# Performance work log

Measured on AMD Instinct MI355X. Metric: run time of the kernel, lower is better.

The kernel has to match this reference:

```python
import jax, jax.numpy as jnp
import numpy as np

B, T_FRAMES, N, D, H, HT = 2, 16, 256, 768, 12, 12
INNER = 2 * D  # ConditionedTransitionBlock expansion_factor=2

def _ln(x, eps=1e-5):
    m = jnp.mean(x, axis=-1, keepdims=True)
    v = jnp.var(x, axis=-1, keepdims=True)
    return (x - m) * jax.lax.rsqrt(v + eps)

def _adaln(a, s, snorm_w, scale_w, scale_b, shift_w):
    an = _ln(a)            # LayerNorm(dim), no affine
    sn = _ln(s) * snorm_w  # LayerNorm(dim_cond), weight only
    return jax.nn.sigmoid(sn @ scale_w + scale_b) * an + sn @ shift_w

def _forward(a, s, bias, timestamps,
             ada_snorm_w, ada_scale_w, ada_scale_b, ada_shift_w,
             pb_q_w, pb_q_b, pb_k_w, pb_v_w, pb_g_w, pb_o_w,
             op_w, op_b,
             tr_snorm_w, tr_scale_w, tr_scale_b, tr_shift_w,
             tr_gate_w, tr_ab_w, tr_ba_w, tr_out_w, tr_out_b,
             tmp_ln_w, tmp_ln_b, tmp_q_w, tmp_q_b, tmp_k_w, tmp_v_w,
             tmp_decay, tmp_o_w,
             mask, multiplicity, T):
    BT, Nn, Dd = a.shape
    Bb = BT // T
    dh = Dd // H
    # --- AdaLN ---
    b = _adaln(a, s, ada_snorm_w, ada_scale_w, ada_scale_b, ada_shift_w)
    # --- pair-bias spatial attention (compute_pair_bias=False: z already (B,N,N,H)) ---
    q = (b @ pb_q_w + pb_q_b).reshape(BT, Nn, H, dh)
    k = (b @ pb_k_w).reshape(BT, Nn, H, dh)
    v = (b @ pb_v_w).reshape(BT, Nn, H, dh)
    z = jnp.transpose(bias, (0, 3, 1, 2))     # (B, H, N, N)
    z = jnp.repeat(z, multiplicity, axis=0)   # expand over T -> (B*T, H, N, N)
    scores = jnp.einsum('bqhd,bkhd->bhqk', q, k) * (dh ** -0.5) + z
    scores = jnp.where(mask[:, None, None, :], scores, -1e6)
    attn = jax.nn.softmax(scores, axis=-1)
    o = jnp.einsum('bhqk,bkhd->bqhd', attn, v).reshape(BT, Nn, Dd)
    g = jax.nn.sigmoid(b @ pb_g_w)
    attn_out = (g * o) @ pb_o_w
    # gated output projection (sigmoid, weights init 0 / bias -2) multiplied into residual
    a = a + jax.nn.sigmoid(s @ op_w + op_b) * attn_out
    # --- temporal attention with decay over T frames ---
    x = a.reshape(Bb, T, Nn, Dd).transpose(0, 2, 1, 3)   # (B, N, T, D)
    h = _ln(x) * tmp_ln_w + tmp_ln_b
    dht = Dd // HT
    qt = (h @ tmp_q_w + tmp_q_b).reshape(Bb, Nn, T, HT, dht)
    kt = (h @ tmp_k_w).reshape(Bb, Nn, T, HT, dht)
    vt = (h @ tmp_v_w).reshape(Bb, Nn, T, HT, dht)
    dt = jnp.abs(timestamps[:, :, None] - timestamps[:, None, :])           # (B, T, T)
    tb = -jax.nn.softplus(tmp_decay)[None, :, None, None] * dt[:, None]     # (B, HT, T, T)
    sct = jnp.einsum('bnqhd,bnkhd->bnhqk', qt, kt) * (dht ** -0.5) + tb[:, None]
    att = jax.nn.softmax(sct, axis=-1)
    ot = jnp.einsum('bnhqk,bnkhd->bnqhd', att, vt).reshape(Bb, Nn, T, Dd) @ tmp_o_w
    x = x + ot  # residual inside temporal attention
    a = x.transpose(0, 2, 1, 3).reshape(BT, Nn, Dd)
    # --- conditioned transition (SwiGLU gated by sigmoid(Linear(s))) ---
    b2 = _adaln(a, s, tr_snorm_w, tr_scale_w, tr_scale_b, tr_shift_w)
    hid = jax.nn.silu(b2 @ tr_gate_w) * (b2 @ tr_ab_w)
    a = a + jax.nn.sigmoid(s @ tr_out_w + tr_out_b) * (hid @ tr_ba_w)
    return a  # post_layer_norm=False -> Identity

def setup_inputs():
    key = jax.random.key(0)
    ks = iter(jax.random.split(key, 48))
    f = lambda shape, sc=1.0: jax.random.normal(next(ks), shape, jnp.float32) * sc
    return {
        'a': f((B * T_FRAMES, N, D)),
        's': f((B * T_FRAMES, N, D)),
        'bias': f((B, N, N, H)),
        'mask': jnp.ones((B * T_FRAMES, N), dtype=bool),
        'timestamps': jnp.sort(jax.random.uniform(next(ks), (B, T_FRAMES)) * 10.0, axis=-1),
        'multiplicity': T_FRAMES,
        'T': T_FRAMES,
        'ada_snorm_w': jnp.ones((D,)), 'ada_scale_w': f((D, D), 0.02),
        'ada_scale_b': jnp.zeros((D,)), 'ada_shift_w': f((D, D), 0.02),
        'pb_q_w': f((D, D), 0.02), 'pb_q_b': jnp.zeros((D,)),
        'pb_k_w': f((D, D), 0.02), 'pb_v_w': f((D, D), 0.02),
        'pb_g_w': f((D, D), 0.02), 'pb_o_w': f((D, D), 0.02),
        'op_w': f((D, D), 0.02), 'op_b': jnp.full((D,), -2.0),
        'tr_snorm_w': jnp.ones((D,)), 'tr_scale_w': f((D, D), 0.02),
        'tr_scale_b': jnp.zeros((D,)), 'tr_shift_w': f((D, D), 0.02),
        'tr_gate_w': f((D, INNER), 0.02), 'tr_ab_w': f((D, INNER), 0.02),
        'tr_ba_w': f((INNER, D), 0.02),
        'tr_out_w': f((D, D), 0.02), 'tr_out_b': jnp.full((D,), -2.0),
        'tmp_ln_w': jnp.ones((D,)), 'tmp_ln_b': jnp.zeros((D,)),
        'tmp_q_w': f((D, D), 0.02), 'tmp_q_b': jnp.zeros((D,)),
        'tmp_k_w': f((D, D), 0.02), 'tmp_v_w': f((D, D), 0.02),
        'tmp_decay': jnp.full((HT,), 0.5), 'tmp_o_w': f((D, D), 0.02),
    }

def reference(a, s, bias, mask, timestamps, multiplicity, T,
              ada_snorm_w, ada_scale_w, ada_scale_b, ada_shift_w,
              pb_q_w, pb_q_b, pb_k_w, pb_v_w, pb_g_w, pb_o_w,
              op_w, op_b,
              tr_snorm_w, tr_scale_w, tr_scale_b, tr_shift_w,
              tr_gate_w, tr_ab_w, tr_ba_w, tr_out_w, tr_out_b,
              tmp_ln_w, tmp_ln_b, tmp_q_w, tmp_q_b, tmp_k_w, tmp_v_w,
              tmp_decay, tmp_o_w):
    return _forward(a, s, bias, timestamps,
                    ada_snorm_w, ada_scale_w, ada_scale_b, ada_shift_w,
                    pb_q_w, pb_q_b, pb_k_w, pb_v_w, pb_g_w, pb_o_w,
                    op_w, op_b,
                    tr_snorm_w, tr_scale_w, tr_scale_b, tr_shift_w,
                    tr_gate_w, tr_ab_w, tr_ba_w, tr_out_w, tr_out_b,
                    tmp_ln_w, tmp_ln_b, tmp_q_w, tmp_q_b, tmp_k_w, tmp_v_w,
                    tmp_decay, tmp_o_w,
                    mask, multiplicity, T)
```

## Files before the change

### kernel.cpp

```cpp
#include <hip/hip_runtime.h>

typedef short s16x8 __attribute__((ext_vector_type(8)));
typedef short s16x4 __attribute__((ext_vector_type(4)));
typedef float f32x4 __attribute__((ext_vector_type(4)));
typedef __bf16 bf16x8 __attribute__((ext_vector_type(8)));

__device__ __forceinline__ float bf2f(short u) {
  union { unsigned int i; float f; } c;
  c.i = ((unsigned int)(unsigned short)u) << 16;
  return c.f;
}
__device__ __forceinline__ short f2bf(float f) {
  union { float f; unsigned int i; } c; c.f = f;
  unsigned int r = c.i + 0x7FFFu + ((c.i >> 16) & 1u);
  return (short)(r >> 16);
}
__device__ __forceinline__ float sigmoidf_(float x) { return 1.f / (1.f + __expf(-x)); }

template <typename T>
__device__ __forceinline__ auto mfma_sel(T a, T b, f32x4 c, int)
    -> decltype(__builtin_amdgcn_mfma_f32_16x16x32_bf16(a, b, c, 0, 0, 0)) {
  return __builtin_amdgcn_mfma_f32_16x16x32_bf16(a, b, c, 0, 0, 0);
}
template <typename T>
__device__ __forceinline__ f32x4 mfma_sel(T a, T b, f32x4 c, long) {
  return __builtin_amdgcn_mfma_f32_16x16x32_bf16(
      __builtin_bit_cast(bf16x8, a), __builtin_bit_cast(bf16x8, b), c, 0, 0, 0);
}
__device__ __forceinline__ f32x4 MFMA16(s16x8 a, s16x8 b, f32x4 c) {
  return mfma_sel(a, b, c, 0);
}

__device__ __forceinline__ void gl2lds16(const void* g, void* l) {
  __builtin_amdgcn_global_load_lds(
      (const __attribute__((address_space(1))) unsigned int*)g,
      (__attribute__((address_space(3))) unsigned int*)l, 16, 0, 0);
}

#define OFF_WADA1    0u
#define OFF_WQKVG    2359296u
#define OFF_WO       7077888u
#define OFF_WGATES   8257536u
#define OFF_WTMPQKV  10616832u
#define OFF_WTMPO    14155776u
#define OFF_WADA2    15335424u
#define OFF_WTRANS   17694720u
#define OFF_WBA      22413312u
#define OFF_BIAS     24772608u
#define OFF_ZT       24812544u
#define OFF_AN1      31104000u
#define OFF_SN1      43686912u
#define OFF_SN2      56269824u
#define OFF_SBF      68852736u
#define OFF_CADA     81435648u
#define OFF_QKVG     106601472u
#define OFF_GATES    156933120u
#define OFF_OGO      182098944u
#define OFF_A1       194681856u

__global__ __launch_bounds__(256) void prep_all(
    const float* p0, const float* p1, const float* p2, const float* p3,
    const float* p4, const float* p5, const float* p6, const float* p7,
    const float* p8, const float* p9, const float* p10, const float* p11,
    const float* p12, const float* p13, const float* p14, const float* p15,
    const float* p16, const float* p17, short* wsb,
    const float* __restrict__ zsrc, const float* __restrict__ ada_scale_b,
    const float* __restrict__ pb_q_b, const float* __restrict__ op_b,
    const float* __restrict__ tr_out_b, const float* __restrict__ tmp_q_b,
    const float* __restrict__ tr_scale_b,
    float* __restrict__ biasbuf, short* __restrict__ zt,
    const float* __restrict__ a_in, const float* __restrict__ s_in,
    const float* __restrict__ lnw1, const float* __restrict__ lnw2,
    short* __restrict__ an1, short* __restrict__ sn1, short* __restrict__ sn2,
    short* __restrict__ sbf) {
  const int z = blockIdx.z;
  const int tid = threadIdx.y * 32 + threadIdx.x;
  if (z < 18) {
    struct E { int K, N, dst; };
    const E tab[18] = {
        {768, 768, 0},        {768, 768, 589824},
        {768, 768, 1179648},  {768, 768, 1769472},
        {768, 768, 2359296},  {768, 768, 2949120},
        {768, 768, 3538944},
        {768, 768, 4128768},  {768, 768, 4718592},
        {768, 768, 7667712},  {768, 768, 8257536},
        {768, 1536, 8847360}, {768, 1536, 10027008},
        {1536, 768, 11206656},
        {768, 768, 5308416},  {768, 768, 5898240}, {768, 768, 6488064},
        {768, 768, 7077888}};
    int K = tab[z].K, N = tab[z].N;
    int n0 = blockIdx.x << 5, k0 = blockIdx.y << 5;
    if (n0 >= N || k0 >= K) return;
    const float* src;
    switch (z) {
      case 0: src = p0; break;  case 1: src = p1; break;
      case 2: src = p2; break;  case 3: src = p3; break;
      case 4: src = p4; break;  case 5: src = p5; break;
      case 6: src = p6; break;  case 7: src = p7; break;
      case 8: src = p8; break;  case 9: src = p9; break;
      case 10: src = p10; break; case 11: src = p11; break;
      case 12: src = p12; break; case 13: src = p13; break;
      case 14: src = p14; break; case 15: src = p15; break;
      case 16: src = p16; break; default: src = p17; break;
    }
    short* dst = wsb + tab[z].dst;
    __shared__ float tile[32][33];
    int tx = threadIdx.x, ty = threadIdx.y;
#pragma unroll
    for (int j = 0; j < 4; j++)
      tile[ty + j * 8][tx] = src[(long)(k0 + ty + j * 8) * N + n0 + tx];
    __syncthreads();
#pragma unroll
    for (int j = 0; j < 4; j++)
      dst[(long)(n0 + ty + j * 8) * K + k0 + tx] = f2bf(tile[tx][ty + j * 8]);
  } else if (z == 18) {
    const int bid = blockIdx.y * 48 + blockIdx.x;
    if (bid < 512) {
      const int b = bid >> 8, qq = bid & 255;
      const float* src = zsrc + (long)bid * 3072 + tid * 12;
      f32x4 v0 = *(const f32x4*)(src);
      f32x4 v1 = *(const f32x4*)(src + 4);
      f32x4 v2 = *(const f32x4*)(src + 8);
      float vals[12] = {v0[0], v0[1], v0[2], v0[3], v1[0], v1[1],
                        v1[2], v1[3], v2[0], v2[1], v2[2], v2[3]};
#pragma unroll
      for (int h = 0; h < 12; h++)
        zt[(((long)(b * 12 + h) * 256 + qq) << 8) + tid] = f2bf(vals[h]);
    } else if (bid < 551) {
      int j = (bid - 512) * 256 + tid;
      if (j < 9984) {
        float v;
        if (j < 1536) v = (j < 768) ? ada_scale_b[j] : 0.f;
        else if (j < 4608) { int jj = j - 1536; v = (jj < 768) ? pb_q_b[jj] : 0.f; }
        else if (j < 6144) { int jj = j - 4608; v = (jj < 768) ? op_b[jj] : tr_out_b[jj - 768]; }
        else if (j < 8448) { int jj = j - 6144; v = (jj < 768) ? tmp_q_b[jj] : 0.f; }
        else { int jj = j - 8448; v = (jj < 768) ? tr_scale_b[jj] : 0.f; }
        biasbuf[j] = v;
      }
    }
  } else {
    const int bid = blockIdx.y * 48 + blockIdx.x;
    if (bid >= 2048) return;
    const int wave = tid >> 6, lane = tid & 63;
    const int row = (bid << 2) + wave;
    const float* ar = a_in + (long)row * 768;
    const float* sr = s_in + (long)row * 768;
    f32x4 av[3], sv[3];
    float s0 = 0, s1 = 0, s2 = 0, s3 = 0;
#pragma unroll
    for (int k = 0; k < 3; k++) {
      int col = (lane << 2) + (k << 8);
      av[k] = *(const f32x4*)(ar + col);
      sv[k] = *(const f32x4*)(sr + col);
#pragma unroll
      for (int e = 0; e < 4; e++) {
        s0 += av[k][e]; s1 += av[k][e] * av[k][e];
        s2 += sv[k][e]; s3 += sv[k][e] * sv[k][e];
      }
    }
#pragma unroll
    for (int o = 32; o; o >>= 1) {
      s0 += __shfl_xor(s0, o, 64); s1 += __shfl_xor(s1, o, 64);
      s2 += __shfl_xor(s2, o, 64); s3 += __shfl_xor(s3, o, 64);
    }
    const float inv768 = 1.f / 768.f;
    float ma = s0 * inv768, va = s1 * inv768 - ma * ma;
    float ia = rsqrtf(va + 1e-5f);
    float ms = s2 * inv768, vs = s3 * inv768 - ms * ms;
    float is_ = rsqrtf(vs + 1e-5f);
#pragma unroll
    for (int k = 0; k < 3; k++) {
      int col = (lane << 2) + (k << 8);
      long o = (long)row * 768 + col;
      s16x4 o1, o2, o3, o4;
#pragma unroll
      for (int e = 0; e < 4; e++) {
        o1[e] = f2bf((av[k][e] - ma) * ia);
        float sn = (sv[k][e] - ms) * is_;
        o2[e] = f2bf(sn * lnw1[col + e]);
        o3[e] = f2bf(sn * lnw2[col + e]);
        o4[e] = f2bf(sv[k][e]);
      }
      *(s16x4*)(an1 + o) = o1;
      *(s16x4*)(sn1 + o) = o2;
      *(s16x4*)(sn2 + o) = o3;
      *(s16x4*)(sbf + o) = o4;
    }
  }
}

__global__ __launch_bounds__(256) void ln_affine(
    const float* __restrict__ in, const float* __restrict__ w,
    const float* __restrict__ b, short* __restrict__ out) {
  const int wave = threadIdx.x >> 6, lane = threadIdx.x & 63;
  const int row = (blockIdx.x << 2) + wave;
  const float* xr = in + (long)row * 768;
  f32x4 xv[3];
  float s0 = 0, s1 = 0;
#pragma unroll
  for (int k = 0; k < 3; k++) {
    int col = (lane << 2) + (k << 8);
    xv[k] = *(const f32x4*)(xr + col);
#pragma unroll
    for (int e = 0; e < 4; e++) { s0 += xv[k][e]; s1 += xv[k][e] * xv[k][e]; }
  }
#pragma unroll
  for (int o = 32; o; o >>= 1) { s0 += __shfl_xor(s0, o, 64); s1 += __shfl_xor(s1, o, 64); }
  const float inv768 = 1.f / 768.f;
  float m = s0 * inv768, v = s1 * inv768 - m * m;
  float inv = rsqrtf(v + 1e-5f);
#pragma unroll
  for (int k = 0; k < 3; k++) {
    int col = (lane << 2) + (k << 8);
    s16x4 p;
#pragma unroll
    for (int e = 0; e < 4; e++) {
      float y = (xv[k][e] - m) * inv;
      if (w) y = y * w[col + e] + b[col + e];
      p[e] = f2bf(y);
    }
    *(s16x4*)(out + (long)row * 768 + col) = p;
  }
}

template <int EP>
__device__ __forceinline__ void dev_gemm_bt(
    short* lds,
    const short* __restrict__ A, const short* __restrict__ W,
    const float* __restrict__ bias, void* __restrict__ Cout,
    const float* __restrict__ res, const short* __restrict__ gate,
    int K, int ldA, int ldC, int gld) {
  short* sA = lds;
  short* sB = lds + 8192;
  const int tid = threadIdx.x;
  const int wave = tid >> 6;
  const int lane = tid & 63;
  const int m0 = blockIdx.y << 7;
  const int n0 = blockIdx.x << 7;
  const int wm = (wave & 1) << 6, wn = (wave >> 1) << 6;
  const int q = lane >> 4, r = lane & 15;
  f32x4 acc[4][4];
#pragma unroll
  for (int i = 0; i < 4; i++)
#pragma unroll
    for (int j = 0; j < 4; j++) acc[i][j] = (f32x4){0.f, 0.f, 0.f, 0.f};

  for (int kt = 0; kt < K; kt += 64) {
    __syncthreads();
#pragma unroll
    for (int t = 0; t < 4; t++) {
      int c = (t << 8) + tid;
      int m = c >> 3, kc = (c & 7) ^ (m & 7);
      gl2lds16(A + (long)(m0 + m) * ldA + kt + (kc << 3),
               sA + (((t << 8) + (wave << 6)) << 3));
    }
#pragma unroll
    for (int t = 0; t < 4; t++) {
      int c = (t << 8) + tid;
      int m = c >> 3, kc = (c & 7) ^ (m & 7);
      gl2lds16(W + (long)(n0 + m) * K + kt + (kc << 3),
               sB + (((t << 8) + (wave << 6)) << 3));
    }
    __syncthreads();
#pragma unroll
    for (int ks = 0; ks < 2; ks++) {
      s16x8 av[4], bv[4];
#pragma unroll
      for (int mt = 0; mt < 4; mt++) {
        int row = wm + (mt << 4) + r;
        int ch = ((ks << 2) + q) ^ (row & 7);
        av[mt] = *(const s16x8*)(sA + ((row << 3) + ch) * 8);
      }
#pragma unroll
      for (int nt = 0; nt < 4; nt++) {
        int row = wn + (nt << 4) + r;
        int ch = ((ks << 2) + q) ^ (row & 7);
        bv[nt] = *(const s16x8*)(sB + ((row << 3) + ch) * 8);
      }
#pragma unroll
      for (int mt = 0; mt < 4; mt++)
#pragma unroll
        for (int nt = 0; nt < 4; nt++)
          acc[mt][nt] = MFMA16(bv[nt], av[mt], acc[mt][nt]);
    }
  }
#pragma unroll
  for (int mt = 0; mt < 4; mt++) {
    const int gm = m0 + wm + (mt << 4) + r;
#pragma unroll
    for (int nt = 0; nt < 4; nt++) {
      const int gnb = n0 + wn + (nt << 4) + (q << 2);
      f32x4 v = acc[mt][nt];
      if (bias) {
        f32x4 b4 = *(const f32x4*)(bias + gnb);
        v += b4;
      }
      long o = (long)gm * ldC + gnb;
      if (EP == 0) {
        s16x4 p;
#pragma unroll
        for (int e = 0; e < 4; e++) p[e] = f2bf(v[e]);
        *(s16x4*)((short*)Cout + o) = p;
      } else if (EP == 1) {
        s16x4 p;
#pragma unroll
        for (int e = 0; e < 4; e++) p[e] = f2bf(sigmoidf_(v[e]));
        *(s16x4*)((short*)Cout + o) = p;
      } else if (EP == 2) {
        f32x4 r4 = *(const f32x4*)(res + o);
        *(f32x4*)((float*)Cout + o) = r4 + v;
      } else {
        f32x4 r4 = *(const f32x4*)(res + o);
        s16x4 g4 = *(const s16x4*)(gate + (long)gm * gld + gnb);
        f32x4 out;
#pragma unroll
        for (int e = 0; e < 4; e++) out[e] = r4[e] + bf2f(g4[e]) * v[e];
        *(f32x4*)((float*)Cout + o) = out;
      }
    }
  }
}

template <int MODE>
__device__ __forceinline__ void dev_gemm_dual(
    short* lds,
    const short* __restrict__ A, const short* __restrict__ W, int woff2,
    const float* __restrict__ bias, const short* __restrict__ an,
    short* __restrict__ out, int ldO) {
  short* sA = lds;
  short* sB1 = lds + 8192;
  short* sB2 = lds + 12288;
  const int tid = threadIdx.x;
  const int wave = tid >> 6, lane = tid & 63;
  const int m0 = blockIdx.y << 7;
  const int n0 = blockIdx.x << 6;
  const int wm = (wave & 1) << 6, wn = (wave >> 1) << 5;
  const int q = lane >> 4, r = lane & 15;
  f32x4 acc1[4][2], acc2[4][2];
#pragma unroll
  for (int i = 0; i < 4; i++)
#pragma unroll
    for (int j = 0; j < 2; j++) {
      acc1[i][j] = (f32x4){0.f, 0.f, 0.f, 0.f};
      acc2[i][j] = (f32x4){0.f, 0.f, 0.f, 0.f};
    }

  for (int kt = 0; kt < 768; kt += 64) {
    __syncthreads();
#pragma unroll
    for (int t = 0; t < 4; t++) {
      int c = (t << 8) + tid;
      int m = c >> 3, kc = (c & 7) ^ (m & 7);
      gl2lds16(A + (long)(m0 + m) * 768 + kt + (kc << 3),
               sA + (((t << 8) + (wave << 6)) << 3));
    }
#pragma unroll
    for (int t = 0; t < 2; t++) {
      int c = (t << 8) + tid;
      int m = c >> 3, kc = (c & 7) ^ (m & 7);
      gl2lds16(W + (long)(n0 + m) * 768 + kt + (kc << 3),
               sB1 + (((t << 8) + (wave << 6)) << 3));
      gl2lds16(W + (long)(woff2 + n0 + m) * 768 + kt + (kc << 3),
               sB2 + (((t << 8) + (wave << 6)) << 3));
    }
    __syncthreads();
#pragma unroll
    for (int ks = 0; ks < 2; ks++) {
      s16x8 av[4], b1[2], b2[2];
#pragma unroll
      for (int mt = 0; mt < 4; mt++) {
        int row = wm + (mt << 4) + r;
        int ch = ((ks << 2) + q) ^ (row & 7);
        av[mt] = *(const s16x8*)(sA + ((row << 3) + ch) * 8);
      }
#pragma unroll
      for (int nt = 0; nt < 2; nt++) {
        int row = wn + (nt << 4) + r;
        int ch = ((ks << 2) + q) ^ (row & 7);
        b1[nt] = *(const s16x8*)(sB1 + ((row << 3) + ch) * 8);
        b2[nt] = *(const s16x8*)(sB2 + ((row << 3) + ch) * 8);
      }
#pragma unroll
      for (int mt = 0; mt < 4; mt++)
#pragma unroll
        for (int nt = 0; nt < 2; nt++) {
          acc1[mt][nt] = MFMA16(b1[nt], av[mt], acc1[mt][nt]);
          acc2[mt][nt] = MFMA16(b2[nt], av[mt], acc2[mt][nt]);
        }
    }
  }
#pragma unroll
  for (int mt = 0; mt < 4; mt++) {
    const int gm = m0 + wm + (mt << 4) + r;
#pragma unroll
    for (int nt = 0; nt < 2; nt++) {
      const int gnb = n0 + wn + (nt << 4) + (q << 2);
      s16x4 p;
      if (MODE == 0) {
        f32x4 b4 = *(const f32x4*)(bias + gnb);
        s16x4 an4 = *(const s16x4*)(an + (long)gm * 768 + gnb);
#pragma unroll
        for (int e = 0; e < 4; e++)
          p[e] = f2bf(sigmoidf_(acc1[mt][nt][e] + b4[e]) * bf2f(an4[e]) +
                      acc2[mt][nt][e]);
      } else {
#pragma unroll
        for (int e = 0; e < 4; e++) {
          float x = acc1[mt][nt][e];
          p[e] = f2bf(x * sigmoidf_(x) * acc2[mt][nt][e]);
        }
      }
      *(s16x4*)(out + (long)gm * ldO + gnb) = p;
    }
  }
}

template <int EP>
__global__ __launch_bounds__(256) void gemm_bt(
    const short* __restrict__ A, const short* __restrict__ W,
    const float* __restrict__ bias, void* __restrict__ Cout,
    const float* __restrict__ res, const short* __restrict__ gate,
    int K, int ldA, int ldC, int gld) {
  __shared__ short lds[16384];
  dev_gemm_bt<EP>(lds, A, W, bias, Cout, res, gate, K, ldA, ldC, gld);
}

template <int MODE>
__global__ __launch_bounds__(256) void gemm_dual(
    const short* __restrict__ A, const short* __restrict__ W, int woff2,
    const float* __restrict__ bias, const short* __restrict__ an,
    short* __restrict__ out, int ldO) {
  __shared__ short lds[16384];
  dev_gemm_dual<MODE>(lds, A, W, woff2, bias, an, out, ldO);
}

__global__ __launch_bounds__(256) void gemm_pair(
    const short* __restrict__ sbf, const short* __restrict__ wgates,
    const float* __restrict__ bias_g, short* __restrict__ gates,
    const short* __restrict__ sn1, const short* __restrict__ wada1,
    const float* __restrict__ bias_a, const short* __restrict__ an1,
    short* __restrict__ outb) {
  __shared__ short lds[16384];
  if (blockIdx.z == 0)
    dev_gemm_bt<1>(lds, sbf, wgates, bias_g, (void*)gates, nullptr, nullptr,
                   768, 768, 1536, 0);
  else
    dev_gemm_dual<0>(lds, sn1, wada1, 768, bias_a, an1, outb, 768);
}

__global__ __launch_bounds__(256) void attn_spatial(
    const short* __restrict__ qkvg, const short* __restrict__ zt, short* __restrict__ ogo) {
  __shared__ short sKP[256 * 64];
  __shared__ short sVt[64 * 256];
  const int tid = threadIdx.x;
  const int wave = tid >> 6, lane = tid & 63;
  const int qt = blockIdx.x, h = blockIdx.y, bt = blockIdx.z;
  const int b = bt >> 4;
  const int q0 = qt << 6;
  const long rowbase = (long)bt << 8;
  const int hoff = h << 6;

#pragma unroll
  for (int t = 0; t < 8; t++) {
    int c = (t << 8) + tid;
    int tok = c >> 3, kc = (c & 7) ^ (tok & 7);
    *(s16x8*)(sKP + (c << 3)) =
        *(const s16x8*)(qkvg + (rowbase + tok) * 3072 + 768 + hoff + (kc << 3));
  }
#pragma unroll
  for (int t = 0; t < 8; t++) {
    int u = (t << 8) + tid;
    int tok = u >> 3, dc = u & 7;
    s16x8 v8 = *(const s16x8*)(qkvg + (rowbase + tok) * 3072 + 1536 + hoff + (dc << 3));
#pragma unroll
    for (int e = 0; e < 8; e++) {
      int d = (dc << 3) + e;
      int ch = (tok >> 3) ^ (d & 7);
      sVt[((d << 5) + ch) * 8 + (tok & 7)] = v8[e];
    }
  }
  __syncthreads();

  const int q = lane >> 4, cc = lane & 15;
  f32x4 acc[16];
#pragma unroll
  for (int i = 0; i < 16; i++) acc[i] = (f32x4){0.f, 0.f, 0.f, 0.f};
  {
    const int arow = (wave << 4) + cc;
    const short* qrow = qkvg + (rowbase + q0 + arow) * 3072 + hoff;
#pragma unroll
    for (int ks = 0; ks < 2; ks++) {
      s16x8 av = *(const s16x8*)(qrow + (ks << 5) + (q << 3));
#pragma unroll
      for (int nt = 0; nt < 16; nt++) {
        int tok = (nt << 4) + cc;
        int chb = ((ks << 2) + q) ^ (tok & 7);
        s16x8 bv = *(const s16x8*)(sKP + ((tok << 3) + chb) * 8);
        acc[nt] = MFMA16(av, bv, acc[nt]);
      }
    }
  }
  const short* ztb = zt + (((long)(b * 12 + h) * 256 + q0 + (wave << 4)) << 8);
#pragma unroll
  for (int reg = 0; reg < 4; reg++) {
    int lr = (q << 2) + reg;
    float mx = -3.0e38f;
#pragma unroll
    for (int nt = 0; nt < 16; nt++) {
      float v = acc[nt][reg] * 0.125f + bf2f(ztb[lr * 256 + (nt << 4) + cc]);
      acc[nt][reg] = v;
      mx = fmaxf(mx, v);
    }
    mx = fmaxf(mx, __shfl_xor(mx, 1, 16));
    mx = fmaxf(mx, __shfl_xor(mx, 2, 16));
    mx = fmaxf(mx, __shfl_xor(mx, 4, 16));
    mx = fmaxf(mx, __shfl_xor(mx, 8, 16));
    float sum = 0.f;
#pragma unroll
    for (int nt = 0; nt < 16; nt++) {
      float e = __expf(acc[nt][reg] - mx);
      acc[nt][reg] = e; sum += e;
    }
    sum += __shfl_xor(sum, 1, 16);
    sum += __shfl_xor(sum, 2, 16);
    sum += __shfl_xor(sum, 4, 16);
    sum += __shfl_xor(sum, 8, 16);
    float inv = 1.f / sum;
#pragma unroll
    for (int nt = 0; nt < 16; nt++) acc[nt][reg] *= inv;
  }
  __syncthreads();
#pragma unroll
  for (int nt = 0; nt < 16; nt++) {
#pragma unroll
    for (int reg = 0; reg < 4; reg++) {
      int rP = (wave << 4) + (q << 2) + reg;
      int col = (nt << 4) + cc;
      int ch = (col >> 3) ^ (rP & 7);
      sKP[((rP << 5) + ch) * 8 + (col & 7)] = f2bf(acc[nt][reg]);
    }
  }
  __syncthreads();
  f32x4 oacc[4];
#pragma unroll
  for (int i = 0; i < 4; i++) oacc[i] = (f32x4){0.f, 0.f, 0.f, 0.f};
  const int prow = (wave << 4) + cc;
#pragma unroll
  for (int ksi = 0; ksi < 8; ksi++) {
    int cha = ((ksi << 2) + q) ^ (prow & 7);
    s16x8 pa = *(const s16x8*)(sKP + ((prow << 5) + cha) * 8);
#pragma unroll
    for (int dt = 0; dt < 4; dt++) {
      int d = (dt << 4) + cc;
      int chv = ((ksi << 2) + q) ^ (d & 7);
      s16x8 bv = *(const s16x8*)(sVt + ((d << 5) + chv) * 8);
      oacc[dt] = MFMA16(pa, bv, oacc[dt]);
    }
  }
#pragma unroll
  for (int dt = 0; dt < 4; dt++) {
#pragma unroll
    for (int reg = 0; reg < 4; reg++) {
      int rowt = q0 + (wave << 4) + (q << 2) + reg;
      int dcol = (dt << 4) + cc;
      long grow = rowbase + rowt;
      float gl = bf2f(qkvg[grow * 3072 + 2304 + hoff + dcol]);
      ogo[grow * 768 + hoff + dcol] = f2bf(oacc[dt][reg] * sigmoidf_(gl));
    }
  }
}

__global__ __launch_bounds__(256) void attn_temporal(
    const short* __restrict__ qkvt, const float* __restrict__ ts,
    const float* __restrict__ decay_raw, short* __restrict__ out) {
  __shared__ short sKV[16 * 1544];
  const int bn = blockIdx.x;
  const int b = bn >> 8, n = bn & 255;
  const int tid = threadIdx.x;
#pragma unroll
  for (int t = 0; t < 12; t++) {
    int u = t * 256 + tid;
    int row = u / 192, cc = u % 192;
    *(s16x8*)(sKV + row * 1544 + cc * 8) =
        *(const s16x8*)(qkvt + ((long)(b * 16 + row) * 256 + n) * 2304 + 768 + cc * 8);
  }
  __syncthreads();
  const int h = tid >> 4, tq = tid & 15;
  if (h < 12) {
    const int hoff = h << 6;
    float dec = log1pf(__expf(decay_raw[h]));
    float tsq = ts[b * 16 + tq];
    s16x8 qv[8];
    const short* qrow = qkvt + ((long)(b * 16 + tq) * 256 + n) * 2304 + hoff;
#pragma unroll
    for (int dc = 0; dc < 8; dc++) qv[dc] = *(const s16x8*)(qrow + dc * 8);
    float sc[16];
#pragma unroll
    for (int tk = 0; tk < 16; tk++) {
      float dot = 0.f;
#pragma unroll
      for (int dc = 0; dc < 8; dc++) {
        s16x8 kv = *(const s16x8*)(sKV + tk * 1544 + hoff + dc * 8);
#pragma unroll
        for (int e = 0; e < 8; e++) dot += bf2f(qv[dc][e]) * bf2f(kv[e]);
      }
      sc[tk] = dot * 0.125f - dec * fabsf(tsq - ts[b * 16 + tk]);
    }
    float mx = sc[0];
#pragma unroll
    for (int tk = 1; tk < 16; tk++) mx = fmaxf(mx, sc[tk]);
    float sum = 0.f;
#pragma unroll
    for (int tk = 0; tk < 16; tk++) { sc[tk] = __expf(sc[tk] - mx); sum += sc[tk]; }
    float inv = 1.f / sum;
    float oa[64];
#pragma unroll
    for (int d = 0; d < 64; d++) oa[d] = 0.f;
#pragma unroll
    for (int tk = 0; tk < 16; tk++) {
      float wgt = sc[tk] * inv;
#pragma unroll
      for (int dc = 0; dc < 8; dc++) {
        s16x8 vv = *(const s16x8*)(sKV + tk * 1544 + 768 + hoff + dc * 8);
#pragma unroll
        for (int e = 0; e < 8; e++) oa[dc * 8 + e] += wgt * bf2f(vv[e]);
      }
    }
    long orow = (long)(b * 16 + tq) * 256 + n;
#pragma unroll
    for (int dc = 0; dc < 8; dc++) {
      s16x8 o8;
#pragma unroll
      for (int e = 0; e < 8; e++) o8[e] = f2bf(oa[dc * 8 + e]);
      *(s16x8*)(out + orow * 768 + hoff + dc * 8) = o8;
    }
  }
}

extern "C" void kernel_launch(void* const* d_in, const int* in_sizes, int n_in,
                              void* d_out, int out_size, void* d_ws, size_t ws_size,
                              hipStream_t stream) {
  (void)in_sizes; (void)n_in; (void)out_size; (void)ws_size;
  const float* a_in      = (const float*)d_in[0];
  const float* s_in      = (const float*)d_in[1];
  const float* bias_in   = (const float*)d_in[2];
  const float* ts        = (const float*)d_in[4];
  const float* ada_snorm = (const float*)d_in[7];
  const float* ada_scale_w = (const float*)d_in[8];
  const float* ada_scale_b = (const float*)d_in[9];
  const float* ada_shift_w = (const float*)d_in[10];
  const float* pb_q_w = (const float*)d_in[11];
  const float* pb_q_b = (const float*)d_in[12];
  const float* pb_k_w = (const float*)d_in[13];
  const float* pb_v_w = (const float*)d_in[14];
  const float* pb_g_w = (const float*)d_in[15];
  const float* pb_o_w = (const float*)d_in[16];
  const float* op_w = (const float*)d_in[17];
  const float* op_b = (const float*)d_in[18];
  const float* tr_snorm = (const float*)d_in[19];
  const float* tr_scale_w = (const float*)d_in[20];
  const float* tr_scale_b = (const float*)d_in[21];
  const float* tr_shift_w = (const float*)d_in[22];
  const float* tr_gate_w = (const float*)d_in[23];
  const float* tr_ab_w = (const float*)d_in[24];
  const float* tr_ba_w = (const float*)d_in[25];
  const float* tr_out_w = (const float*)d_in[26];
  const float* tr_out_b = (const float*)d_in[27];
  const float* tmp_ln_w = (const float*)d_in[28];
  const float* tmp_ln_b = (const float*)d_in[29];
  const float* tmp_q_w = (const float*)d_in[30];
  const float* tmp_q_b = (const float*)d_in[31];
  const float* tmp_k_w = (const float*)d_in[32];
  const float* tmp_v_w = (const float*)d_in[33];
  const float* tmp_decay = (const float*)d_in[34];
  const float* tmp_o_w = (const float*)d_in[35];

  char* ws = (char*)d_ws;
  short* W16 = (short*)ws;
  short* WADA1 = (short*)(ws + OFF_WADA1);
  short* WQKVG = (short*)(ws + OFF_WQKVG);
  short* WO = (short*)(ws + OFF_WO);
  short* WGATES = (short*)(ws + OFF_WGATES);
  short* WTMPQKV = (short*)(ws + OFF_WTMPQKV);
  short* WTMPO = (short*)(ws + OFF_WTMPO);
  short* WADA2 = (short*)(ws + OFF_WADA2);
  short* WTRANS = (short*)(ws + OFF_WTRANS);
  short* WBA = (short*)(ws + OFF_WBA);
  float* BIASB = (float*)(ws + OFF_BIAS);
  short* ZT = (short*)(ws + OFF_ZT);
  short* AN1 = (short*)(ws + OFF_AN1);
  short* SN1 = (short*)(ws + OFF_SN1);
  short* SN2 = (short*)(ws + OFF_SN2);
  short* SBF = (short*)(ws + OFF_SBF);
  short* CADA = (short*)(ws + OFF_CADA);
  short* QKVG = (short*)(ws + OFF_QKVG);
  short* GATES = (short*)(ws + OFF_GATES);
  short* OGO = (short*)(ws + OFF_OGO);
  float* A1F = (float*)(ws + OFF_A1);
  float* OUTF = (float*)d_out;

  prep_all<<<dim3(48, 48, 20), dim3(32, 8, 1), 0, stream>>>(
      ada_scale_w, ada_shift_w, pb_q_w, pb_k_w, pb_v_w, pb_g_w, pb_o_w,
      op_w, tr_out_w, tr_scale_w, tr_shift_w, tr_gate_w, tr_ab_w, tr_ba_w,
      tmp_q_w, tmp_k_w, tmp_v_w, tmp_o_w, W16,
      bias_in, ada_scale_b, pb_q_b, op_b, tr_out_b, tmp_q_b, tr_scale_b,
      BIASB, ZT,
      a_in, s_in, ada_snorm, tr_snorm, AN1, SN1, SN2, SBF);
  gemm_pair<<<dim3(12, 64, 2), 256, 0, stream>>>(
      SBF, WGATES, BIASB + 4608, GATES, SN1, WADA1, BIASB + 0, AN1, SBF);
  gemm_bt<0><<<dim3(24, 64), 256, 0, stream>>>(SBF, WQKVG, BIASB + 1536, QKVG,
                                               nullptr, nullptr, 768, 768, 3072, 0);
  attn_spatial<<<dim3(4, 12, 32), 256, 0, stream>>>(QKVG, ZT, OGO);
  gemm_bt<3><<<dim3(6, 64), 256, 0, stream>>>(OGO, WO, nullptr, A1F, a_in, GATES,
                                              768, 768, 768, 1536);
  ln_affine<<<2048, 256, 0, stream>>>(A1F, tmp_ln_w, tmp_ln_b, AN1);
  gemm_bt<0><<<dim3(18, 64), 256, 0, stream>>>(AN1, WTMPQKV, BIASB + 6144, QKVG,
                                               nullptr, nullptr, 768, 768, 2304, 0);
  attn_temporal<<<512, 256, 0, stream>>>(QKVG, ts, tmp_decay, OGO);
  gemm_bt<2><<<dim3(6, 64), 256, 0, stream>>>(OGO, WTMPO, nullptr, A1F, A1F, nullptr,
                                              768, 768, 768, 0);
  ln_affine<<<2048, 256, 0, stream>>>(A1F, nullptr, nullptr, SN1);
  gemm_dual<0><<<dim3(12, 64), 256, 0, stream>>>(SN2, WADA2, 768, BIASB + 8448, SN1,
                                                 SBF, 768);
  gemm_dual<1><<<dim3(24, 64), 256, 0, stream>>>(SBF, WTRANS, 1536, nullptr, nullptr,
                                                 CADA, 1536);
  gemm_bt<3><<<dim3(6, 64), 256, 0, stream>>>(CADA, WBA, nullptr, OUTF, A1F,
                                              GATES + 768, 1536, 1536, 768, 1536);
}
```

Before: 677.9 us.

## Double-buffer GEMM LDS tiles and remap workgroups across XCDs

```diff
diff --git a/kernel.cpp b/kernel.cpp
--- a/kernel.cpp
+++ b/kernel.cpp
@@ -35,6 +35,12 @@
   __builtin_amdgcn_global_load_lds(
       (const __attribute__((address_space(1))) unsigned int*)g,
       (__attribute__((address_space(3))) unsigned int*)l, 16, 0, 0);
+}
+
+__device__ __forceinline__ int xcd_swz(int id, int nwg) {
+  int q = nwg >> 3, r = nwg & 7;
+  int xcd = id & 7, idx = id >> 3;
+  return (xcd < r ? xcd * (q + 1) : r * (q + 1) + (xcd - r) * q) + idx;
 }
 
 #define OFF_WADA1    0u
@@ -230,13 +236,13 @@
     const float* __restrict__ bias, void* __restrict__ Cout,
     const float* __restrict__ res, const short* __restrict__ gate,
     int K, int ldA, int ldC, int gld) {
-  short* sA = lds;
-  short* sB = lds + 8192;
   const int tid = threadIdx.x;
   const int wave = tid >> 6;
   const int lane = tid & 63;
-  const int m0 = blockIdx.y << 7;
-  const int n0 = blockIdx.x << 7;
+  const int gx = gridDim.x;
+  const int nid = xcd_swz(blockIdx.y * gx + blockIdx.x, gx * gridDim.y);
+  const int m0 = (nid / gx) << 7;
+  const int n0 = (nid % gx) << 7;
   const int wm = (wave & 1) << 6, wn = (wave >> 1) << 6;
   const int q = lane >> 4, r = lane & 15;
   f32x4 acc[4][4];
@@ -245,8 +251,9 @@
 #pragma unroll
     for (int j = 0; j < 4; j++) acc[i][j] = (f32x4){0.f, 0.f, 0.f, 0.f};
 
-  for (int kt = 0; kt < K; kt += 64) {
-    __syncthreads();
+  auto stage = [&](short* buf, int kt) {
+    short* sA = buf;
+    short* sB = buf + 8192;
 #pragma unroll
     for (int t = 0; t < 4; t++) {
       int c = (t << 8) + tid;
@@ -261,7 +268,10 @@
       gl2lds16(W + (long)(n0 + m) * K + kt + (kc << 3),
                sB + (((t << 8) + (wave << 6)) << 3));
     }
-    __syncthreads();
+  };
+  auto compute = [&](const short* buf) {
+    const short* sA = buf;
+    const short* sB = buf + 8192;
 #pragma unroll
     for (int ks = 0; ks < 2; ks++) {
       s16x8 av[4], bv[4];
@@ -283,7 +293,20 @@
         for (int nt = 0; nt < 4; nt++)
           acc[mt][nt] = MFMA16(bv[nt], av[mt], acc[mt][nt]);
     }
-  }
+  };
+
+  short* cb = lds;
+  short* nb = lds + 16384;
+  stage(cb, 0);
+  __syncthreads();
+  for (int kt = 64; kt < K; kt += 64) {
+    stage(nb, kt);
+    compute(cb);
+    __syncthreads();
+    short* t = cb; cb = nb; nb = t;
+  }
+  compute(cb);
+
 #pragma unroll
   for (int mt = 0; mt < 4; mt++) {
     const int gm = m0 + wm + (mt << 4) + r;
@@ -327,13 +350,12 @@
     const short* __restrict__ A, const short* __restrict__ W, int woff2,
     const float* __restrict__ bias, const short* __restrict__ an,
     short* __restrict__ out, int ldO) {
-  short* sA = lds;
-  short* sB1 = lds + 8192;
-  short* sB2 = lds + 12288;
   const int tid = threadIdx.x;
   const int wave = tid >> 6, lane = tid & 63;
-  const int m0 = blockIdx.y << 7;
-  const int n0 = blockIdx.x << 6;
+  const int gx = gridDim.x;
+  const int nid = xcd_swz(blockIdx.y * gx + blockIdx.x, gx * gridDim.y);
+  const int m0 = (nid / gx) << 7;
+  const int n0 = (nid % gx) << 6;
   const int wm = (wave & 1) << 6, wn = (wave >> 1) << 5;
   const int q = lane >> 4, r = lane & 15;
   f32x4 acc1[4][2], acc2[4][2];
@@ -345,8 +367,10 @@
       acc2[i][j] = (f32x4){0.f, 0.f, 0.f, 0.f};
     }
 
-  for (int kt = 0; kt < 768; kt += 64) {
-    __syncthreads();
+  auto stage = [&](short* buf, int kt) {
+    short* sA = buf;
+    short* sB1 = buf + 8192;
+    short* sB2 = buf + 12288;
 #pragma unroll
     for (int t = 0; t < 4; t++) {
       int c = (t << 8) + tid;
@@ -363,7 +387,11 @@
       gl2lds16(W + (long)(woff2 + n0 + m) * 768 + kt + (kc << 3),
                sB2 + (((t << 8) + (wave << 6)) << 3));
     }
-    __syncthreads();
+  };
+  auto compute = [&](const short* buf) {
+    const short* sA = buf;
+    const short* sB1 = buf + 8192;
+    const short* sB2 = buf + 12288;
 #pragma unroll
     for (int ks = 0; ks < 2; ks++) {
       s16x8 av[4], b1[2], b2[2];
@@ -388,7 +416,20 @@
           acc2[mt][nt] = MFMA16(b2[nt], av[mt], acc2[mt][nt]);
         }
     }
-  }
+  };
+
+  short* cb = lds;
+  short* nb = lds + 16384;
+  stage(cb, 0);
+  __syncthreads();
+  for (int kt = 64; kt < 768; kt += 64) {
+    stage(nb, kt);
+    compute(cb);
+    __syncthreads();
+    short* t = cb; cb = nb; nb = t;
+  }
+  compute(cb);
+
 #pragma unroll
   for (int mt = 0; mt < 4; mt++) {
     const int gm = m0 + wm + (mt << 4) + r;
@@ -421,7 +462,7 @@
     const float* __restrict__ bias, void* __restrict__ Cout,
     const float* __restrict__ res, const short* __restrict__ gate,
     int K, int ldA, int ldC, int gld) {
-  __shared__ short lds[16384];
+  __shared__ short lds[32768];
   dev_gemm_bt<EP>(lds, A, W, bias, Cout, res, gate, K, ldA, ldC, gld);
 }
 
@@ -430,7 +471,7 @@
     const short* __restrict__ A, const short* __restrict__ W, int woff2,
     const float* __restrict__ bias, const short* __restrict__ an,
     short* __restrict__ out, int ldO) {
-  __shared__ short lds[16384];
+  __shared__ short lds[32768];
   dev_gemm_dual<MODE>(lds, A, W, woff2, bias, an, out, ldO);
 }
 
@@ -440,7 +481,7 @@
     const short* __restrict__ sn1, const short* __restrict__ wada1,
     const float* __restrict__ bias_a, const short* __restrict__ an1,
     short* __restrict__ outb) {
-  __shared__ short lds[16384];
+  __shared__ short lds[32768];
   if (blockIdx.z == 0)
     dev_gemm_bt<1>(lds, sbf, wgates, bias_g, (void*)gates, nullptr, nullptr,
                    768, 768, 1536, 0);
```

New measurement: 603.7 us. 11.0% less time.
